# Kernel tuning notes

Hardware: AMD Instinct MI355X
Metric: run time of the kernel (lower is better)

Reference implementation:

```python
import jax, jax.numpy as jnp
import numpy as np

THETA = 10000.0
MASK_FILL = -60000.0

def _rope(x):
    # lucidrains rotary_embedding_torch semantics: interleaved pairs, full-dim rotation
    S, D = x.shape[-2], x.shape[-1]
    inv_freq = 1.0 / (THETA ** (jnp.arange(0, D, 2, dtype=jnp.float32) / D))  # [D/2]
    freqs = jnp.arange(S, dtype=jnp.float32)[:, None] * inv_freq[None, :]     # [S, D/2]
    freqs = jnp.repeat(freqs, 2, axis=-1)                                     # [S, D] (each freq twice)
    cos, sin = jnp.cos(freqs), jnp.sin(freqs)
    xr = x.reshape(x.shape[:-1] + (D // 2, 2))
    rot_half = jnp.stack((-xr[..., 1], xr[..., 0]), axis=-1).reshape(x.shape)  # (x1,x2)->(-x2,x1)
    return x * cos + rot_half * sin

def setup_inputs() -> dict:
    key = jax.random.key(0)
    kq, kk, kv, km = jax.random.split(key, 4)
    B, H, S, D = 4, 16, 2048, 128
    return {
        "query": jax.random.normal(kq, (B, H, S, D), dtype=jnp.float32),
        "key": jax.random.normal(kk, (B, H, S, D), dtype=jnp.float32),
        "value": jax.random.normal(kv, (B, H, S, D), dtype=jnp.float32),
        "mask": jax.random.randint(km, (1, 1, S, S), 0, 2, dtype=jnp.int32),
    }

def reference(query, key, value, mask):
    q = _rope(query)
    k = _rope(key)
    scale = 1.0 / jnp.sqrt(jnp.float32(q.shape[-1]))
    scores = jnp.einsum('bhqd,bhkd->bhqk', q, k) * scale
    scores = jnp.where(mask == 0, jnp.float32(MASK_FILL), scores)
    p_attn = jax.nn.softmax(scores, axis=-1)
    out = jnp.einsum('bhqk,bhkd->bhqd', p_attn, value)
    return out, p_attn
```

## Files before the change

kernel.cpp:

```cpp
#include <hip/hip_runtime.h>
#include <hip/hip_fp16.h>
#include <cstdint>
#include <cstddef>

#define Bn 4
#define Hn 16
#define Sn 2048
#define Dn 128
#define MSHIFT 8.0f

typedef _Float16 half8  __attribute__((ext_vector_type(8)));
typedef float    f32x16 __attribute__((ext_vector_type(16)));
typedef float    f32x4v __attribute__((ext_vector_type(4)));
typedef unsigned uint4v __attribute__((ext_vector_type(4)));

__device__ __forceinline__ int pk_f16(float a, float b){
  auto h = __builtin_amdgcn_cvt_pkrtz(a, b);
  return __builtin_bit_cast(int, h);
}


__global__ void k_prep0(float2* __restrict__ tab,
                        const int* __restrict__ mask, unsigned* __restrict__ mtb){
  const int bid = blockIdx.x;
  if (bid < 512){
    const int idx = bid*256 + threadIdx.x;
    const int i = idx & 63, s = idx >> 6;
    const double invf = exp(-(double)i * (9.210340371976184 / 64.0));
    const double ang  = (double)s * invf;
    float2 cs; cs.x = (float)cos(ang); cs.y = (float)sin(ang);
    tab[idx] = cs;
  } else {
    const int g = (bid - 512)*256 + threadIdx.x;
    const int k = g & (Sn-1), q32 = g >> 11;
    unsigned bits = 0u;
    for (int j = 0; j < 32; ++j)
      bits |= (mask[(size_t)(q32*32 + j)*Sn + k] != 0 ? 1u : 0u) << j;
    mtb[g] = bits;
  }
}

__global__ void k_pack_qk(const float* __restrict__ q, const float* __restrict__ k,
                          const float2* __restrict__ tab,
                          half8* __restrict__ qp, half8* __restrict__ kp){
  const int t    = blockIdx.x*256 + threadIdx.x;
  const int lane = t & 63, ln = lane & 31, h = lane >> 5;
  const int dc   = (t >> 6) & 7;
  const int blk  = (t >> 9) & 63;
  const int bh   = t >> 15;
  const int s    = blk*32 + ln;
  const size_t roff = ((size_t)bh*Sn + s)*Dn + dc*16 + h*8;
  const float4 a0 = *(const float4*)(q + roff);
  const float4 a1 = *(const float4*)(q + roff + 4);
  const float4 b0 = *(const float4*)(k + roff);
  const float4 b1 = *(const float4*)(k + roff + 4);
  const float2* tb = tab + s*64 + dc*8 + h*4;
  const float2 c0 = tb[0], c1 = tb[1], c2 = tb[2], c3 = tb[3];
  const float SC = 0.08838834764831845f;
  half8 qo, ko;
  qo[0] = (_Float16)((a0.x*c0.x - a0.y*c0.y)*SC);
  qo[1] = (_Float16)((a0.y*c0.x + a0.x*c0.y)*SC);
  qo[2] = (_Float16)((a0.z*c1.x - a0.w*c1.y)*SC);
  qo[3] = (_Float16)((a0.w*c1.x + a0.z*c1.y)*SC);
  qo[4] = (_Float16)((a1.x*c2.x - a1.y*c2.y)*SC);
  qo[5] = (_Float16)((a1.y*c2.x + a1.x*c2.y)*SC);
  qo[6] = (_Float16)((a1.z*c3.x - a1.w*c3.y)*SC);
  qo[7] = (_Float16)((a1.w*c3.x + a1.z*c3.y)*SC);
  ko[0] = (_Float16)(b0.x*c0.x - b0.y*c0.y);
  ko[1] = (_Float16)(b0.y*c0.x + b0.x*c0.y);
  ko[2] = (_Float16)(b0.z*c1.x - b0.w*c1.y);
  ko[3] = (_Float16)(b0.w*c1.x + b0.z*c1.y);
  ko[4] = (_Float16)(b1.x*c2.x - b1.y*c2.y);
  ko[5] = (_Float16)(b1.y*c2.x + b1.x*c2.y);
  ko[6] = (_Float16)(b1.z*c3.x - b1.w*c3.y);
  ko[7] = (_Float16)(b1.w*c3.x + b1.z*c3.y);
  qp[t] = qo;
  kp[t] = ko;
}

__global__ void k_pack_v(const float* __restrict__ v, half8* __restrict__ vp){
  const int t    = blockIdx.x*256 + threadIdx.x;
  const int lane = t & 63, ln = lane & 31, h = lane >> 5;
  const int dt   = (t >> 6) & 3;
  const int k16  = (t >> 8) & 127;
  const int bh   = t >> 15;
  const size_t base = ((size_t)bh*Sn + k16*16 + h*8)*Dn + dt*32 + ln;
  half8 o;
#pragma unroll
  for (int j = 0; j < 8; ++j) o[j] = (_Float16)v[base + (size_t)j*Dn];
  vp[t] = o;
}


__global__ __launch_bounds__(512, 2) void attn_ps3(
    const half8* __restrict__ qp, const half8* __restrict__ kp,
    const unsigned* __restrict__ mtb, half8* __restrict__ wfrag,
    float* __restrict__ rinvb)
{
  __shared__ float redL[4][2][32];

  const int bid  = blockIdx.x;
  const int work = ((bid & 7) << 7) + (bid >> 3);
  const int w    = threadIdx.x >> 6;
  const int l    = threadIdx.x & 63;
  const int ln   = l & 31;
  const int h    = l >> 5;
  const int sl   = w >> 1;
  const int half = w & 1;
  const int strip = work*4 + sl;
  const int bh   = strip >> 6;
  const int qb   = strip & 63;

  half8 qf[8];
#pragma unroll
  for (int dc = 0; dc < 8; ++dc)
    qf[dc] = qp[(((size_t)bh*64 + qb)*8 + dc)*64 + l];

  const unsigned* mrow = mtb + (size_t)qb*Sn;
  half8* wbase = wfrag + (size_t)strip*128*64;
  float L = 0.f;

  const int kt0 = half*32;
  for (int kt = kt0; kt < kt0 + 32; ++kt){
    const half8* kf = kp + (((size_t)bh*64 + kt)*8)*64 + l;
    f32x16 a;
#pragma unroll
    for (int i = 0; i < 16; ++i) a[i] = 0.f;
#pragma unroll
    for (int dc = 0; dc < 8; ++dc)
      a = __builtin_amdgcn_mfma_f32_32x32x16_f16(kf[(size_t)dc*64], qf[dc], a, 0, 0, 0);

#pragma unroll
    for (int mm = 0; mm < 4; ++mm){
      const uint4v dw = *(const uint4v*)(mrow + kt*32 + mm*8 + h*4);
#pragma unroll
      for (int aa = 0; aa < 4; ++aa){
        const int r = mm*4 + aa;
        const float s = ((dw[aa] >> ln) & 1u) ? a[r] : -1.0e30f;
        const float u = __expf(s - MSHIFT);
        a[r] = u;
        L += u;
      }
    }

    int pk2[4][2];
#pragma unroll
    for (int b = 0; b < 4; ++b){
      pk2[b][0] = pk_f16(a[4*b+0], a[4*b+1]);
      pk2[b][1] = pk_f16(a[4*b+2], a[4*b+3]);
    }

#pragma unroll
    for (int t16 = 0; t16 < 2; ++t16){
      const int P00 = pk2[2*t16+0][0];
      const int P01 = pk2[2*t16+0][1];
      const int P10 = pk2[2*t16+1][0];
      const int P11 = pk2[2*t16+1][1];
      const int S00 = __shfl_xor(P00, 32, 64);
      const int S01 = __shfl_xor(P01, 32, 64);
      const int S10 = __shfl_xor(P10, 32, 64);
      const int S11 = __shfl_xor(P11, 32, 64);
      int4 bi;
      bi.x = h ? S10 : P00;
      bi.y = h ? S11 : P01;
      bi.z = h ? P10 : S00;
      bi.w = h ? P11 : S01;
      wbase[(size_t)(kt*2 + t16)*64 + l] = __builtin_bit_cast(half8, bi);
    }
  }

  L += __shfl_xor(L, 32, 64);
  if (l < 32) redL[sl][half][ln] = L;
  __syncthreads();
  if (half == 0 && l < 32){
    const float Lt = redL[sl][0][ln] + redL[sl][1][ln];
    rinvb[(size_t)strip*32 + ln] = 1.0f / Lt;
  }
}


__global__ __launch_bounds__(512, 2) void attn_o(
    const half8* __restrict__ vp, const half8* __restrict__ wfrag,
    const float* __restrict__ rinvb, float* __restrict__ out)
{
  __shared__ float pt[8][32][34];

  const int bid  = blockIdx.x;
  const int work = 511 - (((bid & 7) << 6) + (bid >> 3));
  const int bh   = work >> 3;
  const int qg   = work & 7;
  const int w    = threadIdx.x >> 6;
  const int l    = threadIdx.x & 63;
  const int ln   = l & 31;
  const int h    = l >> 5;
  const int qb   = qg*8 + w;
  const int strip = bh*64 + qb;

  f32x16 oacc[4];
#pragma unroll
  for (int dt = 0; dt < 4; ++dt)
#pragma unroll
    for (int i = 0; i < 16; ++i) oacc[dt][i] = 0.f;

  const half8* wbase = wfrag + (size_t)strip*128*64;
  const half8* vbase = vp + (size_t)bh*128*4*64;

#pragma unroll 4
  for (int ks = 0; ks < 128; ++ks){
    const half8 bf = wbase[(size_t)ks*64 + l];
    const half8* vf = vbase + (size_t)ks*4*64 + l;
#pragma unroll
    for (int dt = 0; dt < 4; ++dt)
      oacc[dt] = __builtin_amdgcn_mfma_f32_32x32x16_f16(vf[(size_t)dt*64], bf, oacc[dt], 0, 0, 0);
  }

  const float rinv = rinvb[(size_t)strip*32 + ln];
#pragma unroll
  for (int dt = 0; dt < 4; ++dt)
#pragma unroll
    for (int i = 0; i < 16; ++i) oacc[dt][i] *= rinv;

  const size_t obase = ((size_t)bh*Sn + qb*32)*Dn;
  const int rq = l >> 3;
  const int rc = (l & 7) * 4;
#pragma unroll
  for (int dt = 0; dt < 4; ++dt){
#pragma unroll
    for (int g = 0; g < 4; ++g){
      const int c = g*8 + h*4;
      float2 e0, e1;
      e0.x = oacc[dt][4*g+0]; e0.y = oacc[dt][4*g+1];
      e1.x = oacc[dt][4*g+2]; e1.y = oacc[dt][4*g+3];
      *(float2*)&pt[w][ln][c]   = e0;
      *(float2*)&pt[w][ln][c+2] = e1;
    }
#pragma unroll
    for (int i = 0; i < 4; ++i){
      const int qq = i*8 + rq;
      const float2 t0 = *(const float2*)&pt[w][qq][rc];
      const float2 t1 = *(const float2*)&pt[w][qq][rc+2];
      f32x4v o4; o4.x = t0.x; o4.y = t0.y; o4.z = t1.x; o4.w = t1.y;
      __builtin_nontemporal_store(o4, (f32x4v*)(out + obase + (size_t)qq*Dn + dt*32 + rc));
    }
  }
}


__global__ __launch_bounds__(512, 2) void k_expand(
    const half8* __restrict__ wfrag, const float* __restrict__ rinvb,
    float* __restrict__ pout)
{
  __shared__ _Float16 ps[32][1032];
  __shared__ float rv[32];

  const int b     = blockIdx.x;
  const int strip = b >> 1;
  const int hh    = b & 1;
  const int tid   = threadIdx.x;
  const int l     = tid & 63;
  const int w8    = tid >> 6;
  const int ln    = l & 31;
  const int h     = l >> 5;

  if (tid < 32) rv[tid] = rinvb[(size_t)strip*32 + tid];

#pragma unroll
  for (int i = 0; i < 8; ++i){
    const int cc = w8*8 + i;
    const half8 v = wfrag[((size_t)strip*128 + hh*64 + cc)*64 + l];
    *(half8*)&ps[ln][cc*16 + h*8] = v;
  }
  __syncthreads();

  const int bh = strip >> 6, qb = strip & 63;
  float* dst0 = pout + ((size_t)bh*Sn + qb*32)*Sn + hh*1024;
#pragma unroll
  for (int it = 0; it < 8; ++it){
    const int id  = it*512 + tid;
    const int row = id >> 7;
    const int c   = (id & 127) * 8;
    const half8 hv = *(const half8*)&ps[row][c];
    const float r = rv[row];
    f32x4v v0, v1;
    v0.x = (float)hv[0]*r; v0.y = (float)hv[1]*r; v0.z = (float)hv[2]*r; v0.w = (float)hv[3]*r;
    v1.x = (float)hv[4]*r; v1.y = (float)hv[5]*r; v1.z = (float)hv[6]*r; v1.w = (float)hv[7]*r;
    float* dp = dst0 + (size_t)row*Sn + c;
    __builtin_nontemporal_store(v0, (f32x4v*)dp);
    __builtin_nontemporal_store(v1, (f32x4v*)(dp + 4));
  }
}


extern "C" void kernel_launch(void* const* d_in, const int* in_sizes, int n_in,
                              void* d_out, int out_size, void* d_ws, size_t ws_size,
                              hipStream_t stream)
{
  const float* dq = (const float*)d_in[0];
  const float* dk = (const float*)d_in[1];
  const float* dv = (const float*)d_in[2];
  const int*   dm = (const int*)d_in[3];

  char* ws = (char*)d_ws;
  float2*   tab  = (float2*)ws;
  half8*    qp   = (half8*)(ws + (size_t)(1u<<20));
  half8*    kp   = (half8*)(ws + (size_t)(1u<<20) + ((size_t)32<<20));
  half8*    vp   = (half8*)(ws + (size_t)(1u<<20) + ((size_t)64<<20));
  unsigned* mtb  = (unsigned*)(ws + (size_t)(1u<<20) + ((size_t)96<<20));
  float*    rinvb= (float*)(ws + (size_t)(1u<<20) + ((size_t)97<<20));
  half8*    wfr  = (half8*)(ws + (size_t)(1u<<20) + ((size_t)98<<20));

  float* out  = (float*)d_out;
  float* pout = out + (size_t)Bn*Hn*Sn*Dn;

  k_prep0     <<<1024, 256, 0, stream>>>(tab, dm, mtb);
  k_pack_qk   <<<8192, 256, 0, stream>>>(dq, dk, tab, qp, kp);
  k_pack_v    <<<8192, 256, 0, stream>>>(dv, vp);
  attn_ps3    <<<1024, 512, 0, stream>>>(qp, kp, mtb, wfr, rinvb);
  attn_o      <<<512,  512, 0, stream>>>(vp, wfr, rinvb, out);
  k_expand    <<<8192, 512, 0, stream>>>(wfr, rinvb, pout);
}
```

Baseline: 1.036 ms.

## Fuse pack kernels, split attention into two halves, split-K PV with LDS reduction

Merges the Q/K and V packing kernels into one launch, and processes the strips in two halves so the fp16 weight fragments written by attn_ps3 are still cache-resident when attn_o2 and k_expand read them. attn_o2 now gives each pair of waves one strip and splits the 128 k-steps between them. The partial outputs are combined with LDS atomicAdds into a transposed buffer, then written to global memory. The chunking adds launches and the LDS atomic reduction adds shared-memory traffic and barriers. A large zeroed LDS buffer (about 67KB) may also limit occupancy.

```diff
diff --git a/kernel.cpp b/kernel.cpp
--- a/kernel.cpp
+++ b/kernel.cpp
@@ -40,74 +40,76 @@
   }
 }
 
-__global__ void k_pack_qk(const float* __restrict__ q, const float* __restrict__ k,
-                          const float2* __restrict__ tab,
-                          half8* __restrict__ qp, half8* __restrict__ kp){
-  const int t    = blockIdx.x*256 + threadIdx.x;
-  const int lane = t & 63, ln = lane & 31, h = lane >> 5;
-  const int dc   = (t >> 6) & 7;
-  const int blk  = (t >> 9) & 63;
-  const int bh   = t >> 15;
-  const int s    = blk*32 + ln;
-  const size_t roff = ((size_t)bh*Sn + s)*Dn + dc*16 + h*8;
-  const float4 a0 = *(const float4*)(q + roff);
-  const float4 a1 = *(const float4*)(q + roff + 4);
-  const float4 b0 = *(const float4*)(k + roff);
-  const float4 b1 = *(const float4*)(k + roff + 4);
-  const float2* tb = tab + s*64 + dc*8 + h*4;
-  const float2 c0 = tb[0], c1 = tb[1], c2 = tb[2], c3 = tb[3];
-  const float SC = 0.08838834764831845f;
-  half8 qo, ko;
-  qo[0] = (_Float16)((a0.x*c0.x - a0.y*c0.y)*SC);
-  qo[1] = (_Float16)((a0.y*c0.x + a0.x*c0.y)*SC);
-  qo[2] = (_Float16)((a0.z*c1.x - a0.w*c1.y)*SC);
-  qo[3] = (_Float16)((a0.w*c1.x + a0.z*c1.y)*SC);
-  qo[4] = (_Float16)((a1.x*c2.x - a1.y*c2.y)*SC);
-  qo[5] = (_Float16)((a1.y*c2.x + a1.x*c2.y)*SC);
-  qo[6] = (_Float16)((a1.z*c3.x - a1.w*c3.y)*SC);
-  qo[7] = (_Float16)((a1.w*c3.x + a1.z*c3.y)*SC);
-  ko[0] = (_Float16)(b0.x*c0.x - b0.y*c0.y);
-  ko[1] = (_Float16)(b0.y*c0.x + b0.x*c0.y);
-  ko[2] = (_Float16)(b0.z*c1.x - b0.w*c1.y);
-  ko[3] = (_Float16)(b0.w*c1.x + b0.z*c1.y);
-  ko[4] = (_Float16)(b1.x*c2.x - b1.y*c2.y);
-  ko[5] = (_Float16)(b1.y*c2.x + b1.x*c2.y);
-  ko[6] = (_Float16)(b1.z*c3.x - b1.w*c3.y);
-  ko[7] = (_Float16)(b1.w*c3.x + b1.z*c3.y);
-  qp[t] = qo;
-  kp[t] = ko;
-}
-
-__global__ void k_pack_v(const float* __restrict__ v, half8* __restrict__ vp){
-  const int t    = blockIdx.x*256 + threadIdx.x;
-  const int lane = t & 63, ln = lane & 31, h = lane >> 5;
-  const int dt   = (t >> 6) & 3;
-  const int k16  = (t >> 8) & 127;
-  const int bh   = t >> 15;
-  const size_t base = ((size_t)bh*Sn + k16*16 + h*8)*Dn + dt*32 + ln;
-  half8 o;
-#pragma unroll
-  for (int j = 0; j < 8; ++j) o[j] = (_Float16)v[base + (size_t)j*Dn];
-  vp[t] = o;
+__global__ void k_pack(const float* __restrict__ q, const float* __restrict__ k,
+                       const float* __restrict__ v, const float2* __restrict__ tab,
+                       half8* __restrict__ qp, half8* __restrict__ kp,
+                       half8* __restrict__ vp){
+  const int bid = blockIdx.x;
+  if (bid < 8192){
+    const int t    = bid*256 + threadIdx.x;
+    const int lane = t & 63, ln = lane & 31, h = lane >> 5;
+    const int dc   = (t >> 6) & 7;
+    const int blk  = (t >> 9) & 63;
+    const int bh   = t >> 15;
+    const int s    = blk*32 + ln;
+    const size_t roff = ((size_t)bh*Sn + s)*Dn + dc*16 + h*8;
+    const float4 a0 = *(const float4*)(q + roff);
+    const float4 a1 = *(const float4*)(q + roff + 4);
+    const float4 b0 = *(const float4*)(k + roff);
+    const float4 b1 = *(const float4*)(k + roff + 4);
+    const float2* tb = tab + s*64 + dc*8 + h*4;
+    const float2 c0 = tb[0], c1 = tb[1], c2 = tb[2], c3 = tb[3];
+    const float SC = 0.08838834764831845f;
+    half8 qo, ko;
+    qo[0] = (_Float16)((a0.x*c0.x - a0.y*c0.y)*SC);
+    qo[1] = (_Float16)((a0.y*c0.x + a0.x*c0.y)*SC);
+    qo[2] = (_Float16)((a0.z*c1.x - a0.w*c1.y)*SC);
+    qo[3] = (_Float16)((a0.w*c1.x + a0.z*c1.y)*SC);
+    qo[4] = (_Float16)((a1.x*c2.x - a1.y*c2.y)*SC);
+    qo[5] = (_Float16)((a1.y*c2.x + a1.x*c2.y)*SC);
+    qo[6] = (_Float16)((a1.z*c3.x - a1.w*c3.y)*SC);
+    qo[7] = (_Float16)((a1.w*c3.x + a1.z*c3.y)*SC);
+    ko[0] = (_Float16)(b0.x*c0.x - b0.y*c0.y);
+    ko[1] = (_Float16)(b0.y*c0.x + b0.x*c0.y);
+    ko[2] = (_Float16)(b0.z*c1.x - b0.w*c1.y);
+    ko[3] = (_Float16)(b0.w*c1.x + b0.z*c1.y);
+    ko[4] = (_Float16)(b1.x*c2.x - b1.y*c2.y);
+    ko[5] = (_Float16)(b1.y*c2.x + b1.x*c2.y);
+    ko[6] = (_Float16)(b1.z*c3.x - b1.w*c3.y);
+    ko[7] = (_Float16)(b1.w*c3.x + b1.z*c3.y);
+    qp[t] = qo;
+    kp[t] = ko;
+  } else {
+    const int t    = (bid - 8192)*256 + threadIdx.x;
+    const int lane = t & 63, ln = lane & 31, h = lane >> 5;
+    const int dt   = (t >> 6) & 3;
+    const int k16  = (t >> 8) & 127;
+    const int bh   = t >> 15;
+    const size_t base = ((size_t)bh*Sn + k16*16 + h*8)*Dn + dt*32 + ln;
+    half8 o;
+#pragma unroll
+    for (int j = 0; j < 8; ++j) o[j] = (_Float16)v[base + (size_t)j*Dn];
+    vp[t] = o;
+  }
 }
 
 
 __global__ __launch_bounds__(512, 2) void attn_ps3(
     const half8* __restrict__ qp, const half8* __restrict__ kp,
     const unsigned* __restrict__ mtb, half8* __restrict__ wfrag,
-    float* __restrict__ rinvb)
+    float* __restrict__ rinvb, int sbase)
 {
   __shared__ float redL[4][2][32];
 
   const int bid  = blockIdx.x;
-  const int work = ((bid & 7) << 7) + (bid >> 3);
+  const int work = ((bid & 7) << 6) + (bid >> 3);
   const int w    = threadIdx.x >> 6;
   const int l    = threadIdx.x & 63;
   const int ln   = l & 31;
   const int h    = l >> 5;
   const int sl   = w >> 1;
   const int half = w & 1;
-  const int strip = work*4 + sl;
+  const int strip = sbase + work*4 + sl;
   const int bh   = strip >> 6;
   const int qb   = strip & 63;
 
@@ -179,22 +181,23 @@
 }
 
 
-__global__ __launch_bounds__(512, 2) void attn_o(
+__global__ __launch_bounds__(512, 2) void attn_o2(
     const half8* __restrict__ vp, const half8* __restrict__ wfrag,
-    const float* __restrict__ rinvb, float* __restrict__ out)
+    const float* __restrict__ rinvb, float* __restrict__ out, int sbase)
 {
-  __shared__ float pt[8][32][34];
+  __shared__ float lds_out[4][128*33];
 
   const int bid  = blockIdx.x;
   const int work = 511 - (((bid & 7) << 6) + (bid >> 3));
-  const int bh   = work >> 3;
-  const int qg   = work & 7;
-  const int w    = threadIdx.x >> 6;
-  const int l    = threadIdx.x & 63;
+  const int tid  = threadIdx.x;
+  const int w    = tid >> 6;
+  const int l    = tid & 63;
   const int ln   = l & 31;
   const int h    = l >> 5;
-  const int qb   = qg*8 + w;
-  const int strip = bh*64 + qb;
+  const int sl   = w >> 1;
+  const int hf   = w & 1;
+  const int strip = sbase + work*4 + sl;
+  const int bh   = strip >> 6;
 
   f32x16 oacc[4];
 #pragma unroll
@@ -205,8 +208,9 @@
   const half8* wbase = wfrag + (size_t)strip*128*64;
   const half8* vbase = vp + (size_t)bh*128*4*64;
 
+  const int k0 = hf*64;
 #pragma unroll 4
-  for (int ks = 0; ks < 128; ++ks){
+  for (int ks = k0; ks < k0 + 64; ++ks){
     const half8 bf = wbase[(size_t)ks*64 + l];
     const half8* vf = vbase + (size_t)ks*4*64 + l;
 #pragma unroll
@@ -220,41 +224,46 @@
 #pragma unroll
     for (int i = 0; i < 16; ++i) oacc[dt][i] *= rinv;
 
-  const size_t obase = ((size_t)bh*Sn + qb*32)*Dn;
-  const int rq = l >> 3;
-  const int rc = (l & 7) * 4;
+  for (int i = tid; i < 4*128*33; i += 512) ((float*)lds_out)[i] = 0.f;
+  __syncthreads();
 #pragma unroll
   for (int dt = 0; dt < 4; ++dt){
 #pragma unroll
-    for (int g = 0; g < 4; ++g){
-      const int c = g*8 + h*4;
-      float2 e0, e1;
-      e0.x = oacc[dt][4*g+0]; e0.y = oacc[dt][4*g+1];
-      e1.x = oacc[dt][4*g+2]; e1.y = oacc[dt][4*g+3];
-      *(float2*)&pt[w][ln][c]   = e0;
-      *(float2*)&pt[w][ln][c+2] = e1;
+    for (int r = 0; r < 16; ++r){
+      const int d = dt*32 + (r&3) + 8*(r>>2) + h*4;
+      atomicAdd(&lds_out[sl][d*33 + ln], oacc[dt][r]);
     }
-#pragma unroll
-    for (int i = 0; i < 4; ++i){
-      const int qq = i*8 + rq;
-      const float2 t0 = *(const float2*)&pt[w][qq][rc];
-      const float2 t1 = *(const float2*)&pt[w][qq][rc+2];
-      f32x4v o4; o4.x = t0.x; o4.y = t0.y; o4.z = t1.x; o4.w = t1.y;
-      __builtin_nontemporal_store(o4, (f32x4v*)(out + obase + (size_t)qq*Dn + dt*32 + rc));
-    }
+  }
+  __syncthreads();
+
+#pragma unroll
+  for (int it = 0; it < 8; ++it){
+    const int idx = it*512 + tid;
+    const int slx = idx >> 10;
+    const int rem = idx & 1023;
+    const int qq  = rem >> 5;
+    const int c4  = (rem & 31) * 4;
+    const int strip_s = sbase + work*4 + slx;
+    const size_t ob = (((size_t)(strip_s >> 6))*Sn + (strip_s & 63)*32 + qq)*Dn + c4;
+    f32x4v v4;
+    v4.x = lds_out[slx][(c4+0)*33 + qq];
+    v4.y = lds_out[slx][(c4+1)*33 + qq];
+    v4.z = lds_out[slx][(c4+2)*33 + qq];
+    v4.w = lds_out[slx][(c4+3)*33 + qq];
+    __builtin_nontemporal_store(v4, (f32x4v*)(out + ob));
   }
 }
 
 
 __global__ __launch_bounds__(512, 2) void k_expand(
     const half8* __restrict__ wfrag, const float* __restrict__ rinvb,
-    float* __restrict__ pout)
+    float* __restrict__ pout, int sbase)
 {
   __shared__ _Float16 ps[32][1032];
   __shared__ float rv[32];
 
   const int b     = blockIdx.x;
-  const int strip = b >> 1;
+  const int strip = sbase + (b >> 1);
   const int hh    = b & 1;
   const int tid   = threadIdx.x;
   const int l     = tid & 63;
@@ -312,10 +321,12 @@
   float* out  = (float*)d_out;
   float* pout = out + (size_t)Bn*Hn*Sn*Dn;
 
-  k_prep0     <<<1024, 256, 0, stream>>>(tab, dm, mtb);
-  k_pack_qk   <<<8192, 256, 0, stream>>>(dq, dk, tab, qp, kp);
-  k_pack_v    <<<8192, 256, 0, stream>>>(dv, vp);
-  attn_ps3    <<<1024, 512, 0, stream>>>(qp, kp, mtb, wfr, rinvb);
-  attn_o      <<<512,  512, 0, stream>>>(vp, wfr, rinvb, out);
-  k_expand    <<<8192, 512, 0, stream>>>(wfr, rinvb, pout);
-}
+  k_prep0 <<<1024,  256, 0, stream>>>(tab, dm, mtb);
+  k_pack  <<<16384, 256, 0, stream>>>(dq, dk, dv, tab, qp, kp, vp);
+  for (int c = 0; c < 2; ++c){
+    const int sbase = c*2048;
+    attn_ps3 <<<512,  512, 0, stream>>>(qp, kp, mtb, wfr, rinvb, sbase);
+    attn_o2  <<<512,  512, 0, stream>>>(vp, wfr, rinvb, out, sbase);
+    k_expand <<<4096, 512, 0, stream>>>(wfr, rinvb, pout, sbase);
+  }
+}
```

Result: slower. 1.138 ms (+9.9%).
